# Performance work log

Measured on AMD Instinct MI355X. Metric: run time of the kernel, lower is better.

## Reference

```python
import jax, jax.numpy as jnp
import numpy as np

GAMMA = 2.0  # focal focusing parameter
LAM = 0.1    # disco weight


def _centered_dist(x, nw):
    """Doubly (weighted) centered pairwise |x_i - x_j| matrix, as in distance_corr."""
    d = jnp.abs(x[:, None] - x[None, :])          # [N, N]
    davg = jnp.mean(d * nw, axis=1)               # [N]  (row-wise weighted mean)
    return d - davg[None, :] - davg[:, None] + jnp.mean(davg * nw)


def _dcorr(Amat, Bmat, nw):
    ABavg = jnp.mean(Amat * Bmat * nw, axis=1)
    AAavg = jnp.mean(Amat * Amat * nw, axis=1)
    BBavg = jnp.mean(Bmat * Bmat * nw, axis=1)
    return jnp.mean(ABavg * nw) / jnp.sqrt(jnp.mean(AAavg * nw) * jnp.mean(BBavg * nw))


def setup_inputs() -> dict:
    key = jax.random.key(0)
    k1, k2, k3, k4 = jax.random.split(key, 4)
    N, C = 8192, 4
    return {
        "outputs": jax.random.normal(k1, (N, C), dtype=jnp.float32),
        "labels": jax.random.randint(k2, (N,), 0, C, dtype=jnp.int32),
        "event": jax.random.normal(k3, (N,), dtype=jnp.float32),
        "weights": jax.random.uniform(k4, (N, 1), dtype=jnp.float32, minval=0.1, maxval=1.0),
    }


def reference(outputs, labels, event, weights):
    N, C = outputs.shape
    w = weights.squeeze()                          # [N]

    # Focal loss (reduction='none'), alpha=None
    logp = jax.nn.log_softmax(outputs, axis=1)     # [N, C]
    logpt = logp[jnp.arange(N), labels]            # [N]
    pt = jnp.exp(logpt)
    focal = -(1.0 - pt) ** GAMMA * logpt * w       # per-example, times weights

    probs = jnp.exp(logp)                          # softmax(outputs)
    nw = w * N / jnp.sum(w)                        # normed weights (sum == N)

    # event-side centered distance matrix is class-independent: compute once
    Bmat = _centered_dist(event, nw)               # [N, N]

    disco = jnp.float32(0.0)
    for i in range(C):                             # small fixed class loop
        Amat = _centered_dist(probs[:, i], nw)
        disco = disco + _dcorr(Amat, Bmat, nw)
    disco = disco / C

    f = jnp.mean(focal)
    return jnp.stack([f, disco, f + LAM * disco])  # [focal, disco, tot]
```

## Files before the change

kernel.cpp:

```cpp
#include <hip/hip_runtime.h>
#include <math.h>

#define BLK 256
#define JSPLIT 16
#define LAM 0.1f

__device__ __forceinline__ float wave_reduce(float v) {
    v += __shfl_down(v, 32, 64);
    v += __shfl_down(v, 16, 64);
    v += __shfl_down(v, 8, 64);
    v += __shfl_down(v, 4, 64);
    v += __shfl_down(v, 2, 64);
    v += __shfl_down(v, 1, 64);
    return v;
}

__global__ __launch_bounds__(BLK) void k1_rowprep(
        const float* __restrict__ outs, const int* __restrict__ labels,
        const float* __restrict__ wts, float* __restrict__ probs,
        float* __restrict__ scal) {
    __shared__ float lds[8];
    int i = blockIdx.x * BLK + threadIdx.x;
    float4 o = ((const float4*)outs)[i];
    float m = fmaxf(fmaxf(o.x, o.y), fmaxf(o.z, o.w));
    float e0 = expf(o.x - m), e1 = expf(o.y - m), e2 = expf(o.z - m), e3 = expf(o.w - m);
    float s = e0 + e1 + e2 + e3;
    float inv = 1.0f / s;
    float4 p = make_float4(e0 * inv, e1 * inv, e2 * inv, e3 * inv);
    ((float4*)probs)[i] = p;
    int l = labels[i];
    float ol = (l == 0) ? o.x : (l == 1) ? o.y : (l == 2) ? o.z : o.w;
    float logpt = ol - m - logf(s);
    float pt = expf(logpt);
    float w = wts[i];
    float om = 1.0f - pt;
    float focal = -om * om * logpt * w;

    int lane = threadIdx.x & 63, wave = threadIdx.x >> 6;
    float fr = wave_reduce(focal);
    if (lane == 0) lds[wave] = fr;
    __syncthreads();
    if (threadIdx.x == 0) atomicAdd(&scal[9], lds[0] + lds[1] + lds[2] + lds[3]);
    __syncthreads();
    float wr = wave_reduce(w);
    if (lane == 0) lds[wave] = wr;
    __syncthreads();
    if (threadIdx.x == 0) atomicAdd(&scal[10], lds[0] + lds[1] + lds[2] + lds[3]);
}

__global__ __launch_bounds__(BLK) void k2_pairs(
        const float* __restrict__ probs, const float* __restrict__ event,
        const float* __restrict__ wts, float* __restrict__ rows,
        float* __restrict__ scal, int N) {
    __shared__ float4 jp[BLK];
    __shared__ float2 jew[BLK];
    __shared__ float red[4][9];

    int tid = threadIdx.x;
    int i = blockIdx.x * BLK + tid;
    float4 pi = ((const float4*)probs)[i];
    float ei = event[i];
    float wi = wts[i];

    int jcount = N / JSPLIT;
    int jbase = blockIdx.y * jcount;

    float s0 = 0.f, s1 = 0.f, s2 = 0.f, s3 = 0.f, se = 0.f;
    float t0e = 0.f, t1e = 0.f, t2e = 0.f, t3e = 0.f, tee = 0.f;
    float t00 = 0.f, t11 = 0.f, t22 = 0.f, t33 = 0.f;

    for (int jc = 0; jc < jcount; jc += BLK) {
        int j = jbase + jc + tid;
        jp[tid] = ((const float4*)probs)[j];
        jew[tid] = make_float2(event[j], wts[j]);
        __syncthreads();
#pragma unroll 4
        for (int jj = 0; jj < BLK; ++jj) {
            float4 p = jp[jj];
            float2 ew = jew[jj];
            float d0 = fabsf(pi.x - p.x);
            float d1 = fabsf(pi.y - p.y);
            float d2 = fabsf(pi.z - p.z);
            float d3 = fabsf(pi.w - p.w);
            float de = fabsf(ei - ew.x);
            float wj = ew.y;
            s0 = fmaf(wj, d0, s0);
            s1 = fmaf(wj, d1, s1);
            s2 = fmaf(wj, d2, s2);
            s3 = fmaf(wj, d3, s3);
            se = fmaf(wj, de, se);
            float wde = wj * de;
            t0e = fmaf(wde, d0, t0e);
            t1e = fmaf(wde, d1, t1e);
            t2e = fmaf(wde, d2, t2e);
            t3e = fmaf(wde, d3, t3e);
            tee = fmaf(wde, de, tee);
            float wd0 = wj * d0, wd1 = wj * d1, wd2 = wj * d2, wd3 = wj * d3;
            t00 = fmaf(wd0, d0, t00);
            t11 = fmaf(wd1, d1, t11);
            t22 = fmaf(wd2, d2, t22);
            t33 = fmaf(wd3, d3, t33);
        }
        __syncthreads();
    }

    atomicAdd(&rows[0 * N + i], s0);
    atomicAdd(&rows[1 * N + i], s1);
    atomicAdd(&rows[2 * N + i], s2);
    atomicAdd(&rows[3 * N + i], s3);
    atomicAdd(&rows[4 * N + i], se);

    float t[9] = {t0e * wi, t1e * wi, t2e * wi, t3e * wi, tee * wi,
                  t00 * wi, t11 * wi, t22 * wi, t33 * wi};
    int lane = tid & 63, wave = tid >> 6;
#pragma unroll
    for (int k = 0; k < 9; ++k) t[k] = wave_reduce(t[k]);
    if (lane == 0) {
#pragma unroll
        for (int k = 0; k < 9; ++k) red[wave][k] = t[k];
    }
    __syncthreads();
    if (tid < 9)
        atomicAdd(&scal[tid], red[0][tid] + red[1][tid] + red[2][tid] + red[3][tid]);
}

__global__ __launch_bounds__(BLK) void k3_final(
        const float* __restrict__ rows, const float* __restrict__ scal,
        const float* __restrict__ wts, float* __restrict__ out, int N) {
    float acc[14];
#pragma unroll
    for (int k = 0; k < 14; ++k) acc[k] = 0.f;

    for (int i = threadIdx.x; i < N; i += BLK) {
        float w = wts[i];
        float s0 = rows[0 * N + i], s1 = rows[1 * N + i], s2 = rows[2 * N + i],
              s3 = rows[3 * N + i], sE = rows[4 * N + i];
        acc[0] += w * s0; acc[1] += w * s1; acc[2] += w * s2;
        acc[3] += w * s3; acc[4] += w * sE;
        float wE = w * sE;
        acc[5] += wE * s0; acc[6] += wE * s1; acc[7] += wE * s2; acc[8] += wE * s3;
        acc[9] += wE * sE;
        acc[10] += w * s0 * s0; acc[11] += w * s1 * s1;
        acc[12] += w * s2 * s2; acc[13] += w * s3 * s3;
    }

    __shared__ float red[4][14];
    int lane = threadIdx.x & 63, wave = threadIdx.x >> 6;
#pragma unroll
    for (int k = 0; k < 14; ++k) acc[k] = wave_reduce(acc[k]);
    if (lane == 0) {
#pragma unroll
        for (int k = 0; k < 14; ++k) red[wave][k] = acc[k];
    }
    __syncthreads();

    if (threadIdx.x == 0) {
        float SW[5], SWW_ce[4], SWW_ee, SWW_cc[4];
#pragma unroll
        for (int k = 0; k < 5; ++k) SW[k] = red[0][k] + red[1][k] + red[2][k] + red[3][k];
#pragma unroll
        for (int k = 0; k < 4; ++k) SWW_ce[k] = red[0][5 + k] + red[1][5 + k] + red[2][5 + k] + red[3][5 + k];
        SWW_ee = red[0][9] + red[1][9] + red[2][9] + red[3][9];
#pragma unroll
        for (int k = 0; k < 4; ++k) SWW_cc[k] = red[0][10 + k] + red[1][10 + k] + red[2][10 + k] + red[3][10 + k];

        float W = scal[10];
        float invW2 = 1.0f / (W * W);
        float invW3 = invW2 / W;

        float g0 = SW[0] * invW2, g1 = SW[1] * invW2, g2 = SW[2] * invW2,
              g3 = SW[3] * invW2, gE = SW[4] * invW2;

        float num_ee = scal[4] * invW2 - 2.0f * SWW_ee * invW3 + gE * gE;
        float gc[4] = {g0, g1, g2, g3};
        float disco = 0.f;
#pragma unroll
        for (int c = 0; c < 4; ++c) {
            float num_ce = scal[c] * invW2 - 2.0f * SWW_ce[c] * invW3 + gc[c] * gE;
            float num_cc = scal[5 + c] * invW2 - 2.0f * SWW_cc[c] * invW3 + gc[c] * gc[c];
            disco += num_ce * rsqrtf(num_cc * num_ee);
        }
        disco *= 0.25f;

        float f = scal[9] / (float)N;
        out[0] = f;
        out[1] = disco;
        out[2] = f + LAM * disco;
    }
}

extern "C" void kernel_launch(void* const* d_in, const int* in_sizes, int n_in,
                              void* d_out, int out_size, void* d_ws, size_t ws_size,
                              hipStream_t stream) {
    const float* outs = (const float*)d_in[0];
    const int* labels = (const int*)d_in[1];
    const float* event = (const float*)d_in[2];
    const float* wts = (const float*)d_in[3];
    float* out = (float*)d_out;
    int N = in_sizes[1];

    float* ws = (float*)d_ws;
    float* probs = ws;
    float* rows = ws + (size_t)N * 4;
    float* scal = rows + (size_t)N * 5;

    hipMemsetAsync(rows, 0, ((size_t)N * 5 + 11) * sizeof(float), stream);

    k1_rowprep<<<N / BLK, BLK, 0, stream>>>(outs, labels, wts, probs, scal);

    dim3 g2(N / BLK, JSPLIT);
    k2_pairs<<<g2, BLK, 0, stream>>>(probs, event, wts, rows, scal, N);

    k3_final<<<1, BLK, 0, stream>>>(rows, scal, wts, out, N);
}
```

Measured before the change: 126.9 us.

## Compute squared-distance sums in closed form and register-tile two rows per thread

The per-pair squared self-distance terms (t00..t33, tee) are dropped from the O(N^2) inner loop and recovered from weighted first and second moments computed in the prep kernel (sum_ij w_i w_j (x_i-x_j)^2 = 2(W*M2 - M1^2)). Each thread now handles two i rows, reusing every LDS j load twice, and the j split is doubled to keep the grid size unchanged. The memset is replaced by zeroing inside the prep kernel, and per-block partials go to a buffer that a 1024-thread final kernel reduces. The moment identity can lose float precision through cancellation, and the extra per-thread accumulators raise register pressure.

Result: faster. 113.2 us (-10.8%).

```diff
diff --git a/kernel.cpp b/kernel.cpp
--- a/kernel.cpp
+++ b/kernel.cpp
@@ -2,8 +2,10 @@
 #include <math.h>
 
 #define BLK 256
-#define JSPLIT 16
+#define IT 2
+#define JSPLIT 32
 #define LAM 0.1f
+
 
 __device__ __forceinline__ float wave_reduce(float v) {
     v += __shfl_down(v, 32, 64);
@@ -17,9 +19,10 @@
 
 __global__ __launch_bounds__(BLK) void k1_rowprep(
         const float* __restrict__ outs, const int* __restrict__ labels,
-        const float* __restrict__ wts, float* __restrict__ probs,
-        float* __restrict__ scal) {
-    __shared__ float lds[8];
+        const float* __restrict__ event, const float* __restrict__ wts,
+        float* __restrict__ probs, float* __restrict__ rows,
+        float* __restrict__ scal, float* __restrict__ kpart, int N) {
+    __shared__ float red[4][12];
     int i = blockIdx.x * BLK + threadIdx.x;
     float4 o = ((const float4*)outs)[i];
     float m = fmaxf(fmaxf(o.x, o.y), fmaxf(o.z, o.w));
@@ -28,24 +31,34 @@
     float inv = 1.0f / s;
     float4 p = make_float4(e0 * inv, e1 * inv, e2 * inv, e3 * inv);
     ((float4*)probs)[i] = p;
+
     int l = labels[i];
     float ol = (l == 0) ? o.x : (l == 1) ? o.y : (l == 2) ? o.z : o.w;
     float logpt = ol - m - logf(s);
     float pt = expf(logpt);
     float w = wts[i];
+    float ev = event[i];
     float om = 1.0f - pt;
     float focal = -om * om * logpt * w;
 
+#pragma unroll
+    for (int v = 0; v < 5; ++v) rows[v * N + i] = 0.f;
+    if (blockIdx.x == 0 && threadIdx.x < 4) scal[threadIdx.x] = 0.f;
+
+    float vals[12] = {focal, w,
+                      w * p.x, w * p.y, w * p.z, w * p.w, w * ev,
+                      w * p.x * p.x, w * p.y * p.y, w * p.z * p.z,
+                      w * p.w * p.w, w * ev * ev};
     int lane = threadIdx.x & 63, wave = threadIdx.x >> 6;
-    float fr = wave_reduce(focal);
-    if (lane == 0) lds[wave] = fr;
+#pragma unroll
+    for (int k = 0; k < 12; ++k) {
+        float r = wave_reduce(vals[k]);
+        if (lane == 0) red[wave][k] = r;
+    }
     __syncthreads();
-    if (threadIdx.x == 0) atomicAdd(&scal[9], lds[0] + lds[1] + lds[2] + lds[3]);
-    __syncthreads();
-    float wr = wave_reduce(w);
-    if (lane == 0) lds[wave] = wr;
-    __syncthreads();
-    if (threadIdx.x == 0) atomicAdd(&scal[10], lds[0] + lds[1] + lds[2] + lds[3]);
+    if (threadIdx.x < 12)
+        kpart[blockIdx.x * 12 + threadIdx.x] =
+            red[0][threadIdx.x] + red[1][threadIdx.x] + red[2][threadIdx.x] + red[3][threadIdx.x];
 }
 
 __global__ __launch_bounds__(BLK) void k2_pairs(
@@ -54,20 +67,23 @@
         float* __restrict__ scal, int N) {
     __shared__ float4 jp[BLK];
     __shared__ float2 jew[BLK];
-    __shared__ float red[4][9];
+    __shared__ float red[4][4];
 
     int tid = threadIdx.x;
-    int i = blockIdx.x * BLK + tid;
-    float4 pi = ((const float4*)probs)[i];
-    float ei = event[i];
-    float wi = wts[i];
+    int i0 = blockIdx.x * (BLK * IT) + tid;
+    int i1 = i0 + BLK;
+    float4 pA = ((const float4*)probs)[i0];
+    float4 pB = ((const float4*)probs)[i1];
+    float eA = event[i0], eB = event[i1];
+    float wA = wts[i0], wB = wts[i1];
 
     int jcount = N / JSPLIT;
     int jbase = blockIdx.y * jcount;
 
-    float s0 = 0.f, s1 = 0.f, s2 = 0.f, s3 = 0.f, se = 0.f;
-    float t0e = 0.f, t1e = 0.f, t2e = 0.f, t3e = 0.f, tee = 0.f;
-    float t00 = 0.f, t11 = 0.f, t22 = 0.f, t33 = 0.f;
+    float sA0 = 0.f, sA1 = 0.f, sA2 = 0.f, sA3 = 0.f, sAe = 0.f;
+    float sB0 = 0.f, sB1 = 0.f, sB2 = 0.f, sB3 = 0.f, sBe = 0.f;
+    float tA0 = 0.f, tA1 = 0.f, tA2 = 0.f, tA3 = 0.f;
+    float tB0 = 0.f, tB1 = 0.f, tB2 = 0.f, tB3 = 0.f;
 
     for (int jc = 0; jc < jcount; jc += BLK) {
         int j = jbase + jc + tid;
@@ -78,60 +94,94 @@
         for (int jj = 0; jj < BLK; ++jj) {
             float4 p = jp[jj];
             float2 ew = jew[jj];
-            float d0 = fabsf(pi.x - p.x);
-            float d1 = fabsf(pi.y - p.y);
-            float d2 = fabsf(pi.z - p.z);
-            float d3 = fabsf(pi.w - p.w);
-            float de = fabsf(ei - ew.x);
             float wj = ew.y;
-            s0 = fmaf(wj, d0, s0);
-            s1 = fmaf(wj, d1, s1);
-            s2 = fmaf(wj, d2, s2);
-            s3 = fmaf(wj, d3, s3);
-            se = fmaf(wj, de, se);
-            float wde = wj * de;
-            t0e = fmaf(wde, d0, t0e);
-            t1e = fmaf(wde, d1, t1e);
-            t2e = fmaf(wde, d2, t2e);
-            t3e = fmaf(wde, d3, t3e);
-            tee = fmaf(wde, de, tee);
-            float wd0 = wj * d0, wd1 = wj * d1, wd2 = wj * d2, wd3 = wj * d3;
-            t00 = fmaf(wd0, d0, t00);
-            t11 = fmaf(wd1, d1, t11);
-            t22 = fmaf(wd2, d2, t22);
-            t33 = fmaf(wd3, d3, t33);
+            {
+                float d0 = fabsf(pA.x - p.x);
+                float d1 = fabsf(pA.y - p.y);
+                float d2 = fabsf(pA.z - p.z);
+                float d3 = fabsf(pA.w - p.w);
+                float de = fabsf(eA - ew.x);
+                sA0 = fmaf(wj, d0, sA0);
+                sA1 = fmaf(wj, d1, sA1);
+                sA2 = fmaf(wj, d2, sA2);
+                sA3 = fmaf(wj, d3, sA3);
+                sAe = fmaf(wj, de, sAe);
+                float wde = wj * de;
+                tA0 = fmaf(wde, d0, tA0);
+                tA1 = fmaf(wde, d1, tA1);
+                tA2 = fmaf(wde, d2, tA2);
+                tA3 = fmaf(wde, d3, tA3);
+            }
+            {
+                float d0 = fabsf(pB.x - p.x);
+                float d1 = fabsf(pB.y - p.y);
+                float d2 = fabsf(pB.z - p.z);
+                float d3 = fabsf(pB.w - p.w);
+                float de = fabsf(eB - ew.x);
+                sB0 = fmaf(wj, d0, sB0);
+                sB1 = fmaf(wj, d1, sB1);
+                sB2 = fmaf(wj, d2, sB2);
+                sB3 = fmaf(wj, d3, sB3);
+                sBe = fmaf(wj, de, sBe);
+                float wde = wj * de;
+                tB0 = fmaf(wde, d0, tB0);
+                tB1 = fmaf(wde, d1, tB1);
+                tB2 = fmaf(wde, d2, tB2);
+                tB3 = fmaf(wde, d3, tB3);
+            }
         }
         __syncthreads();
     }
 
-    atomicAdd(&rows[0 * N + i], s0);
-    atomicAdd(&rows[1 * N + i], s1);
-    atomicAdd(&rows[2 * N + i], s2);
-    atomicAdd(&rows[3 * N + i], s3);
-    atomicAdd(&rows[4 * N + i], se);
-
-    float t[9] = {t0e * wi, t1e * wi, t2e * wi, t3e * wi, tee * wi,
-                  t00 * wi, t11 * wi, t22 * wi, t33 * wi};
+    atomicAdd(&rows[0 * N + i0], sA0);
+    atomicAdd(&rows[1 * N + i0], sA1);
+    atomicAdd(&rows[2 * N + i0], sA2);
+    atomicAdd(&rows[3 * N + i0], sA3);
+    atomicAdd(&rows[4 * N + i0], sAe);
+    atomicAdd(&rows[0 * N + i1], sB0);
+    atomicAdd(&rows[1 * N + i1], sB1);
+    atomicAdd(&rows[2 * N + i1], sB2);
+    atomicAdd(&rows[3 * N + i1], sB3);
+    atomicAdd(&rows[4 * N + i1], sBe);
+
+    float t0 = tA0 * wA + tB0 * wB;
+    float t1 = tA1 * wA + tB1 * wB;
+    float t2 = tA2 * wA + tB2 * wB;
+    float t3 = tA3 * wA + tB3 * wB;
     int lane = tid & 63, wave = tid >> 6;
-#pragma unroll
-    for (int k = 0; k < 9; ++k) t[k] = wave_reduce(t[k]);
+    t0 = wave_reduce(t0); t1 = wave_reduce(t1);
+    t2 = wave_reduce(t2); t3 = wave_reduce(t3);
     if (lane == 0) {
-#pragma unroll
-        for (int k = 0; k < 9; ++k) red[wave][k] = t[k];
+        red[wave][0] = t0; red[wave][1] = t1;
+        red[wave][2] = t2; red[wave][3] = t3;
     }
     __syncthreads();
-    if (tid < 9)
+    if (tid < 4)
         atomicAdd(&scal[tid], red[0][tid] + red[1][tid] + red[2][tid] + red[3][tid]);
 }
 
-__global__ __launch_bounds__(BLK) void k3_final(
+__global__ __launch_bounds__(1024) void k3_final(
         const float* __restrict__ rows, const float* __restrict__ scal,
-        const float* __restrict__ wts, float* __restrict__ out, int N) {
+        const float* __restrict__ wts, const float* __restrict__ kpart,
+        float* __restrict__ out, int N) {
+    __shared__ float red[16][14];
+    __shared__ float fin[12];
+    int tid = threadIdx.x, lane = tid & 63, wave = tid >> 6;
+
+    if (wave == 0) {
+#pragma unroll
+        for (int k = 0; k < 12; ++k) {
+            float v = (lane < 32) ? kpart[lane * 12 + k] : 0.f;
+            v = wave_reduce(v);
+            if (lane == 0) fin[k] = v;
+        }
+    }
+
     float acc[14];
 #pragma unroll
     for (int k = 0; k < 14; ++k) acc[k] = 0.f;
 
-    for (int i = threadIdx.x; i < N; i += BLK) {
+    for (int i = tid; i < N; i += 1024) {
         float w = wts[i];
         float s0 = rows[0 * N + i], s1 = rows[1 * N + i], s2 = rows[2 * N + i],
               s3 = rows[3 * N + i], sE = rows[4 * N + i];
@@ -144,8 +194,6 @@
         acc[12] += w * s2 * s2; acc[13] += w * s3 * s3;
     }
 
-    __shared__ float red[4][14];
-    int lane = threadIdx.x & 63, wave = threadIdx.x >> 6;
 #pragma unroll
     for (int k = 0; k < 14; ++k) acc[k] = wave_reduce(acc[k]);
     if (lane == 0) {
@@ -154,35 +202,59 @@
     }
     __syncthreads();
 
-    if (threadIdx.x == 0) {
+    if (tid == 0) {
         float SW[5], SWW_ce[4], SWW_ee, SWW_cc[4];
 #pragma unroll
-        for (int k = 0; k < 5; ++k) SW[k] = red[0][k] + red[1][k] + red[2][k] + red[3][k];
-#pragma unroll
-        for (int k = 0; k < 4; ++k) SWW_ce[k] = red[0][5 + k] + red[1][5 + k] + red[2][5 + k] + red[3][5 + k];
-        SWW_ee = red[0][9] + red[1][9] + red[2][9] + red[3][9];
-#pragma unroll
-        for (int k = 0; k < 4; ++k) SWW_cc[k] = red[0][10 + k] + red[1][10 + k] + red[2][10 + k] + red[3][10 + k];
-
-        float W = scal[10];
+        for (int k = 0; k < 5; ++k) {
+            float a = 0.f;
+            for (int wv = 0; wv < 16; ++wv) a += red[wv][k];
+            SW[k] = a;
+        }
+#pragma unroll
+        for (int k = 0; k < 4; ++k) {
+            float a = 0.f;
+            for (int wv = 0; wv < 16; ++wv) a += red[wv][5 + k];
+            SWW_ce[k] = a;
+        }
+        {
+            float a = 0.f;
+            for (int wv = 0; wv < 16; ++wv) a += red[wv][9];
+            SWW_ee = a;
+        }
+#pragma unroll
+        for (int k = 0; k < 4; ++k) {
+            float a = 0.f;
+            for (int wv = 0; wv < 16; ++wv) a += red[wv][10 + k];
+            SWW_cc[k] = a;
+        }
+
+        float focal_sum = fin[0];
+        float W = fin[1];
+        float M1[5] = {fin[2], fin[3], fin[4], fin[5], fin[6]};
+        float M2[5] = {fin[7], fin[8], fin[9], fin[10], fin[11]};
+
         float invW2 = 1.0f / (W * W);
         float invW3 = invW2 / W;
 
-        float g0 = SW[0] * invW2, g1 = SW[1] * invW2, g2 = SW[2] * invW2,
-              g3 = SW[3] * invW2, gE = SW[4] * invW2;
-
-        float num_ee = scal[4] * invW2 - 2.0f * SWW_ee * invW3 + gE * gE;
-        float gc[4] = {g0, g1, g2, g3};
+        float g[5];
+#pragma unroll
+        for (int v = 0; v < 5; ++v) g[v] = SW[v] * invW2;
+        float gE = g[4];
+
+        float Tee = 2.0f * (W * M2[4] - M1[4] * M1[4]);
+        float num_ee = Tee * invW2 - 2.0f * SWW_ee * invW3 + gE * gE;
+
         float disco = 0.f;
 #pragma unroll
         for (int c = 0; c < 4; ++c) {
-            float num_ce = scal[c] * invW2 - 2.0f * SWW_ce[c] * invW3 + gc[c] * gE;
-            float num_cc = scal[5 + c] * invW2 - 2.0f * SWW_cc[c] * invW3 + gc[c] * gc[c];
+            float Tcc = 2.0f * (W * M2[c] - M1[c] * M1[c]);
+            float num_cc = Tcc * invW2 - 2.0f * SWW_cc[c] * invW3 + g[c] * g[c];
+            float num_ce = scal[c] * invW2 - 2.0f * SWW_ce[c] * invW3 + g[c] * gE;
             disco += num_ce * rsqrtf(num_cc * num_ee);
         }
         disco *= 0.25f;
 
-        float f = scal[9] / (float)N;
+        float f = focal_sum / (float)N;
         out[0] = f;
         out[1] = disco;
         out[2] = f + LAM * disco;
@@ -201,15 +273,14 @@
 
     float* ws = (float*)d_ws;
     float* probs = ws;
-    float* rows = ws + (size_t)N * 4;
+    float* rows = probs + (size_t)N * 4;
     float* scal = rows + (size_t)N * 5;
-
-    hipMemsetAsync(rows, 0, ((size_t)N * 5 + 11) * sizeof(float), stream);
-
-    k1_rowprep<<<N / BLK, BLK, 0, stream>>>(outs, labels, wts, probs, scal);
-
-    dim3 g2(N / BLK, JSPLIT);
+    float* kpart = scal + 16;
+
+    k1_rowprep<<<N / BLK, BLK, 0, stream>>>(outs, labels, event, wts, probs, rows, scal, kpart, N);
+
+    dim3 g2(N / (BLK * IT), JSPLIT);
     k2_pairs<<<g2, BLK, 0, stream>>>(probs, event, wts, rows, scal, N);
 
-    k3_final<<<1, BLK, 0, stream>>>(rows, scal, wts, out, N);
-}
+    k3_final<<<1, 1024, 0, stream>>>(rows, scal, wts, kpart, out, N);
+}
```
